# Optimization experiments

Measured on AMD Instinct MI355X. Metric: run time of the kernel, lower is better.

The kernel has to match this reference:

```python
import jax, jax.numpy as jnp
import numpy as np

B, S, D, H = 2, 2048, 2048, 16
HD = D // H  # head_dim = 128


def setup_inputs() -> dict:
    key = jax.random.key(0)
    ks = jax.random.split(key, 9)
    s = 1.0 / np.sqrt(D)
    return {
        "x": jax.random.normal(ks[0], (B, S, D), jnp.float32),
        "Wq": jax.random.normal(ks[1], (D, D), jnp.float32) * s,
        "bq": jax.random.normal(ks[2], (D,), jnp.float32) * 0.02,
        "Wk": jax.random.normal(ks[3], (D, D), jnp.float32) * s,
        "bk": jax.random.normal(ks[4], (D,), jnp.float32) * 0.02,
        "Wv": jax.random.normal(ks[5], (D, D), jnp.float32) * s,
        "bv": jax.random.normal(ks[6], (D,), jnp.float32) * 0.02,
        "Wo": jax.random.normal(ks[7], (D, D), jnp.float32) * s,
        "bo": jax.random.normal(ks[8], (D,), jnp.float32) * 0.02,
    }


def reference(x, Wq, bq, Wk, bk, Wv, bv, Wo, bo):
    b, s, d = x.shape
    # nn.Linear: y = x @ W.T + b
    def split(t):
        # [b, s, d] -> [b, H, s, HD]
        return t.reshape(b, s, H, HD).transpose(0, 2, 1, 3)

    q = split(x @ Wq.T + bq)
    k = split(x @ Wk.T + bk)
    v = split(x @ Wv.T + bv)

    scale = jnp.asarray(HD, x.dtype) ** 0.5
    qk = jnp.einsum("bhqd,bhkd->bhqk", q, k) / scale  # [b, H, s, s]
    weights = jax.nn.softmax(qk, axis=-1)
    attn = jnp.einsum("bhqk,bhkd->bhqd", weights, v)  # [b, H, s, HD]

    merged = attn.transpose(0, 2, 1, 3).reshape(b, s, d)
    return merged @ Wo.T + bo
```

## Files before the change

### kernel.cpp

```cpp
#include <hip/hip_runtime.h>

typedef __bf16 bf16_t;
typedef bf16_t bf16x8 __attribute__((ext_vector_type(8)));
typedef bf16_t bf16x4 __attribute__((ext_vector_type(4)));
typedef float  f32x4  __attribute__((ext_vector_type(4)));

#define DDIM  2048
#define SEQ   2048
#define NH    16
#define HDIM  128
#define BATCH 2
#define MROWS (BATCH * SEQ)
#define XEL   ((size_t)MROWS * DDIM)

__device__ __forceinline__ void async_ld16(const bf16_t* g, bf16_t* l) {
  __builtin_amdgcn_global_load_lds(
      (const __attribute__((address_space(1))) void*)g,
      (__attribute__((address_space(3))) void*)l, 16, 0, 0);
}

__global__ void cvt_f32_bf16(const float* __restrict__ in,
                             bf16_t* __restrict__ out, int n) {
  int i = (blockIdx.x * blockDim.x + threadIdx.x) * 4;
  const int stride = gridDim.x * blockDim.x * 4;
  for (; i < n; i += stride) {
    const float4 v = *reinterpret_cast<const float4*>(in + i);
    bf16x4 o;
    o[0] = (bf16_t)v.x; o[1] = (bf16_t)v.y;
    o[2] = (bf16_t)v.z; o[3] = (bf16_t)v.w;
    *reinterpret_cast<bf16x4*>(out + i) = o;
  }
}

__global__ __launch_bounds__(512, 2) void gemm_qkv(
    const bf16_t* __restrict__ Ax, const bf16_t* __restrict__ Wcat,
    const float* __restrict__ bq, const float* __restrict__ bk,
    const float* __restrict__ bv,
    bf16_t* __restrict__ QKVh, float qscale) {
  __shared__ __align__(16) bf16_t sA[2][2][128 * 64];
  __shared__ __align__(16) bf16_t sB[2][192 * 64];

  const int tid  = threadIdx.x;
  const int lane = tid & 63;
  const int w    = tid >> 6;
  const int wm   = w >> 2;
  const int wn   = w & 3;
  const int lg   = lane >> 4;
  const int lr   = lane & 15;

  const int bid = blockIdx.x;
  const int l   = (bid & 7) * 64 + (bid >> 3);
  const int tm  = l & 15;
  const int tn  = l >> 4;
  const int row0  = tm * 256;
  const int ncol0 = tn * 192;

  auto stA = [&](int buf, int ha, int kt) {
#pragma unroll
    for (int L = 0; L < 2; ++L) {
      const int c = L * 512 + tid, r = c >> 3, ch = c & 7;
      async_ld16(Ax + (size_t)(row0 + ha * 128 + r) * DDIM + kt * 64 +
                     ((ch ^ (r & 7)) * 8),
                 &sA[buf][ha][c * 8]);
    }
  };
  auto stB = [&](int buf, int kt) {
#pragma unroll
    for (int L = 0; L < 3; ++L) {
      const int c = L * 512 + tid, r = c >> 3, ch = c & 7;
      async_ld16(Wcat + (size_t)(ncol0 + r) * DDIM + kt * 64 +
                     ((ch ^ (r & 7)) * 8),
                 &sB[buf][c * 8]);
    }
  };
  auto ldA = [&](int buf, int mf, int k) {
    const int row = mf * 16 + lr;
    const int ch  = (k * 4 + lg) ^ (row & 7);
    return *reinterpret_cast<const bf16x8*>(&sA[buf][wm][row * 64 + ch * 8]);
  };
  auto ldB = [&](int buf, int nf, int k) {
    const int row = wn * 48 + nf * 16 + lr;
    const int ch  = (k * 4 + lg) ^ (row & 7);
    return *reinterpret_cast<const bf16x8*>(&sB[buf][row * 64 + ch * 8]);
  };

  f32x4  acc[8][3] = {};
  bf16x8 bfr[3][2];

#define GPH(BUF, Q, LOADB, STAGE_STMT, VMW)                                   \
  {                                                                           \
    bf16x8 a00 = ldA(BUF, 2 * (Q), 0), a01 = ldA(BUF, 2 * (Q), 1);            \
    bf16x8 a10 = ldA(BUF, 2 * (Q) + 1, 0), a11 = ldA(BUF, 2 * (Q) + 1, 1);    \
    if (LOADB) {                                                              \
      _Pragma("unroll") for (int nf = 0; nf < 3; ++nf) {                      \
        bfr[nf][0] = ldB(BUF, nf, 0);                                         \
        bfr[nf][1] = ldB(BUF, nf, 1);                                         \
      }                                                                       \
    }                                                                         \
    STAGE_STMT;                                                               \
    if (VMW) asm volatile("s_waitcnt vmcnt(3)" ::: "memory");                 \
    __builtin_amdgcn_s_barrier();                                             \
    asm volatile("s_waitcnt lgkmcnt(0)" ::: "memory");                        \
    __builtin_amdgcn_sched_barrier(0);                                        \
    __builtin_amdgcn_s_setprio(1);                                            \
    _Pragma("unroll") for (int k = 0; k < 2; ++k) {                           \
      const bf16x8 A0 = k ? a01 : a00;                                        \
      const bf16x8 A1 = k ? a11 : a10;                                        \
      _Pragma("unroll") for (int nf = 0; nf < 3; ++nf) {                      \
        acc[2 * (Q)][nf] = __builtin_amdgcn_mfma_f32_16x16x32_bf16(           \
            A0, bfr[nf][k], acc[2 * (Q)][nf], 0, 0, 0);                       \
        acc[2 * (Q) + 1][nf] = __builtin_amdgcn_mfma_f32_16x16x32_bf16(       \
            A1, bfr[nf][k], acc[2 * (Q) + 1][nf], 0, 0, 0);                   \
      }                                                                       \
    }                                                                         \
    __builtin_amdgcn_s_setprio(0);                                            \
    __builtin_amdgcn_s_barrier();                                             \
  }

  stA(0, 0, 0); stA(0, 1, 0);
  stB(0, 0);
  stB(1, 1);
  asm volatile("s_waitcnt vmcnt(3)" ::: "memory");
  __builtin_amdgcn_s_barrier();

  for (int i = 0; i < 16; ++i) {
    const int t1 = (2 * i + 1) & 31;
    const int t2 = (2 * i + 2) & 31;
    const int t3 = (2 * i + 3) & 31;
    GPH(0, 0, true,  { stA(1, 0, t1); stA(1, 1, t1); }, 0)
    GPH(0, 1, false, { stB(0, t2); },                   0)
    GPH(0, 2, false, {},                                0)
    GPH(0, 3, false, {},                                1)
    GPH(1, 0, true,  { stA(0, 0, t2); stA(0, 1, t2); }, 0)
    GPH(1, 1, false, { stB(1, t3); },                   0)
    GPH(1, 2, false, {},                                0)
    GPH(1, 3, false, {},                                1)
  }
#undef GPH
  asm volatile("s_waitcnt vmcnt(0)" ::: "memory");

#pragma unroll
  for (int mf = 0; mf < 8; ++mf) {
    const int rr0 = row0 + wm * 128 + mf * 16 + lg * 4;
#pragma unroll
    for (int nf = 0; nf < 3; ++nf) {
      const int col = ncol0 + wn * 48 + nf * 16 + lr;
      const int mat = col >> 11;
      const int c2  = col & (DDIM - 1);
      const float bs = ((mat == 0) ? bq : (mat == 1) ? bk : bv)[c2];
      const float sc = (mat == 0) ? qscale : 1.0f;
      const int h = c2 >> 7, hd = c2 & (HDIM - 1);
      bf16_t* outb = QKVh + (size_t)mat * XEL;
#pragma unroll
      for (int r = 0; r < 4; ++r) {
        const int rr = rr0 + r;
        const int b = rr >> 11, s = rr & (SEQ - 1);
        outb[(((size_t)(b * NH + h)) * SEQ + s) * HDIM + hd] =
            (bf16_t)((acc[mf][nf][r] + bs) * sc);
      }
    }
  }
}

template <int OUTMODE>
__global__ __launch_bounds__(256) void gemm_bt(
    const bf16_t* __restrict__ A, const bf16_t* __restrict__ Bw,
    const float* __restrict__ bias, void* __restrict__ outp,
    int M, int N, int K, float scale) {
  __shared__ __align__(16) bf16_t sA[2][128 * 32];
  __shared__ __align__(16) bf16_t sB[2][128 * 32];

  const int tid  = threadIdx.x;
  const int lane = tid & 63;
  const int w    = tid >> 6;
  const int wm   = w >> 1;
  const int wn   = w & 1;
  const int lg   = lane >> 4;
  const int lr   = lane & 15;
  const int row0 = blockIdx.y * 128;
  const int col0 = blockIdx.x * 128;

  const int srow = tid >> 2;
  const int scol = (tid & 3) * 8;

  const bf16_t* gA = A  + (size_t)(row0 + srow) * K + scol;
  const bf16_t* gB = Bw + (size_t)(col0 + srow) * K + scol;

  f32x4 acc[4][4] = {};

  auto stage = [&](int buf, int k0) {
    async_ld16(gA + k0,                  &sA[buf][tid * 8]);
    async_ld16(gA + 64 * (size_t)K + k0, &sA[buf][(256 + tid) * 8]);
    async_ld16(gB + k0,                  &sB[buf][tid * 8]);
    async_ld16(gB + 64 * (size_t)K + k0, &sB[buf][(256 + tid) * 8]);
  };

  stage(0, 0);
  __syncthreads();

  int cur = 0;
  const int NT = K / 32;
  for (int t = 0; t < NT; ++t) {
    if (t + 1 < NT) stage(cur ^ 1, (t + 1) * 32);
    bf16x8 af[4], bfr[4];
#pragma unroll
    for (int i = 0; i < 4; ++i) {
      af[i]  = *reinterpret_cast<const bf16x8*>(
          &sA[cur][(wm * 64 + i * 16 + lr) * 32 + lg * 8]);
      bfr[i] = *reinterpret_cast<const bf16x8*>(
          &sB[cur][(wn * 64 + i * 16 + lr) * 32 + lg * 8]);
    }
#pragma unroll
    for (int i = 0; i < 4; ++i)
#pragma unroll
      for (int j = 0; j < 4; ++j)
        acc[i][j] = __builtin_amdgcn_mfma_f32_16x16x32_bf16(
            af[i], bfr[j], acc[i][j], 0, 0, 0);
    __syncthreads();
    cur ^= 1;
  }

#pragma unroll
  for (int i = 0; i < 4; ++i) {
    const int rowb = row0 + wm * 64 + i * 16 + lg * 4;
#pragma unroll
    for (int j = 0; j < 4; ++j) {
      const int col = col0 + wn * 64 + j * 16 + lr;
      const float bs = bias[col];
#pragma unroll
      for (int r = 0; r < 4; ++r) {
        const float v = (acc[i][j][r] + bs) * scale;
        const int rr = rowb + r;
        if (OUTMODE == 2) {
          ((float*)outp)[(size_t)rr * N + col] = v;
        } else {
          const int b  = rr >> 11;
          const int s  = rr & (SEQ - 1);
          const int h  = col >> 7;
          const int hd = col & (HDIM - 1);
          ((bf16_t*)outp)[(((size_t)(b * NH + h)) * SEQ + s) * HDIM + hd] =
              (bf16_t)v;
        }
      }
    }
  }
}

__global__ __launch_bounds__(256) void transpose_v(
    const bf16_t* __restrict__ Vp, bf16_t* __restrict__ Vt) {
  __shared__ __align__(16) bf16_t tt[64][72];
  const int bh = blockIdx.z;
  const int s0 = blockIdx.x * 64;
  const int d0 = blockIdx.y * 64;
  const int t  = threadIdx.x;
#pragma unroll
  for (int c = 0; c < 2; ++c) {
    const int r   = (c * 256 + t) >> 3;
    const int col = (t & 7) * 8;
    bf16x8 v = *reinterpret_cast<const bf16x8*>(
        Vp + ((size_t)bh * SEQ + s0 + r) * HDIM + d0 + col);
    *reinterpret_cast<bf16x8*>(&tt[r][col]) = v;
  }
  __syncthreads();
#pragma unroll
  for (int c = 0; c < 2; ++c) {
    const int dr = (c * 256 + t) >> 3;
    const int sc = (t & 7) * 8;
    bf16x8 o;
#pragma unroll
    for (int i = 0; i < 8; ++i) o[i] = tt[sc + i][dr];
    *reinterpret_cast<bf16x8*>(
        Vt + ((size_t)bh * HDIM + d0 + dr) * SEQ + s0 + sc) = o;
  }
}

__global__ __launch_bounds__(256) void attn_fwd(
    const bf16_t* __restrict__ Q, const bf16_t* __restrict__ K,
    const bf16_t* __restrict__ Vt, bf16_t* __restrict__ out) {
  __shared__ __align__(16) bf16_t sK[64 * 128];
  __shared__ __align__(16) bf16_t sV[128 * 64];
  __shared__ __align__(16) bf16_t sP[4][32][72];

  const int tid  = threadIdx.x;
  const int lane = tid & 63;
  const int w    = tid >> 6;
  const int lg   = lane >> 4;
  const int lr   = lane & 15;

  const int bid     = blockIdx.x;
  const int logical = (bid & 7) * 64 + (bid >> 3);
  const int bh      = logical >> 4;
  const int q0      = (logical & 15) * 128;
  const int qw      = q0 + w * 32;

  const bf16_t* Kb = K  + (size_t)bh * SEQ * HDIM;
  const bf16_t* Vb = Vt + (size_t)bh * HDIM * SEQ;

  bf16x8 qf[2][4];
#pragma unroll
  for (int mf = 0; mf < 2; ++mf) {
    const bf16_t* qbase = Q + ((size_t)bh * SEQ + qw + mf * 16 + lr) * HDIM;
#pragma unroll
    for (int kc = 0; kc < 4; ++kc)
      qf[mf][kc] = *reinterpret_cast<const bf16x8*>(qbase + kc * 32 + lg * 8);
  }

  bf16x8 onesf;
#pragma unroll
  for (int i = 0; i < 8; ++i) onesf[i] = (bf16_t)1.0f;

  f32x4 o[2][8] = {};
  f32x4 o1[2] = {};

  for (int kv0 = 0; kv0 < SEQ; kv0 += 64) {
    __syncthreads();
#pragma unroll
    for (int p = 0; p < 4; ++p) {
      const int slot = p * 256 + tid;
      const int kr = slot >> 4, kc = slot & 15;
      async_ld16(Kb + ((size_t)(kv0 + kr)) * HDIM + ((kc ^ (kr & 7)) * 8),
                 sK + slot * 8);
      const int vr = slot >> 3, vc = slot & 7;
      async_ld16(Vb + (size_t)vr * SEQ + kv0 + ((vc ^ (vr & 7)) * 8),
                 sV + slot * 8);
    }
    __syncthreads();

    f32x4 s[2][4] = {};
    __builtin_amdgcn_s_setprio(1);
#pragma unroll
    for (int kc = 0; kc < 4; ++kc) {
#pragma unroll
      for (int cb = 0; cb < 4; ++cb) {
        const int r  = cb * 16 + lr;
        const int ch = kc * 4 + lg;
        bf16x8 kf = *reinterpret_cast<const bf16x8*>(
            sK + r * 128 + ((ch ^ (r & 7)) * 8));
        s[0][cb] = __builtin_amdgcn_mfma_f32_16x16x32_bf16(qf[0][kc], kf, s[0][cb], 0, 0, 0);
        s[1][cb] = __builtin_amdgcn_mfma_f32_16x16x32_bf16(qf[1][kc], kf, s[1][cb], 0, 0, 0);
      }
    }
    __builtin_amdgcn_s_setprio(0);

#pragma unroll
    for (int mf = 0; mf < 2; ++mf)
#pragma unroll
      for (int r = 0; r < 4; ++r)
#pragma unroll
        for (int cb = 0; cb < 4; ++cb) {
          const float p = __builtin_amdgcn_exp2f(s[mf][cb][r]);
          sP[w][mf * 16 + lg * 4 + r][cb * 16 + lr] = (bf16_t)p;
        }

    asm volatile("s_waitcnt lgkmcnt(0)" ::: "memory");

    __builtin_amdgcn_s_setprio(1);
#pragma unroll
    for (int ks = 0; ks < 2; ++ks) {
      bf16x8 pf0 = *reinterpret_cast<const bf16x8*>(&sP[w][lr][ks * 32 + lg * 8]);
      bf16x8 pf1 = *reinterpret_cast<const bf16x8*>(&sP[w][16 + lr][ks * 32 + lg * 8]);
      o1[0] = __builtin_amdgcn_mfma_f32_16x16x32_bf16(pf0, onesf, o1[0], 0, 0, 0);
      o1[1] = __builtin_amdgcn_mfma_f32_16x16x32_bf16(pf1, onesf, o1[1], 0, 0, 0);
#pragma unroll
      for (int ob = 0; ob < 8; ++ob) {
        const int r  = ob * 16 + lr;
        const int ch = ks * 4 + lg;
        bf16x8 vf = *reinterpret_cast<const bf16x8*>(
            sV + r * 64 + ((ch ^ (r & 7)) * 8));
        o[0][ob] = __builtin_amdgcn_mfma_f32_16x16x32_bf16(pf0, vf, o[0][ob], 0, 0, 0);
        o[1][ob] = __builtin_amdgcn_mfma_f32_16x16x32_bf16(pf1, vf, o[1][ob], 0, 0, 0);
      }
    }
    __builtin_amdgcn_s_setprio(0);
  }

  const int b = bh >> 4, h = bh & 15;
#pragma unroll
  for (int mf = 0; mf < 2; ++mf) {
#pragma unroll
    for (int r = 0; r < 4; ++r) {
      const float inv_l = 1.0f / o1[mf][r];
      const int row = qw + mf * 16 + lg * 4 + r;
      bf16_t* obase = out + ((size_t)b * SEQ + row) * DDIM + h * HDIM;
#pragma unroll
      for (int ob = 0; ob < 8; ++ob)
        obase[ob * 16 + lr] = (bf16_t)(o[mf][ob][r] * inv_l);
    }
  }
}

extern "C" void kernel_launch(void* const* d_in, const int* in_sizes, int n_in,
                              void* d_out, int out_size, void* d_ws,
                              size_t ws_size, hipStream_t stream) {
  const float* x  = (const float*)d_in[0];
  const float* Wq = (const float*)d_in[1];
  const float* bq = (const float*)d_in[2];
  const float* Wk = (const float*)d_in[3];
  const float* bk = (const float*)d_in[4];
  const float* Wv = (const float*)d_in[5];
  const float* bv = (const float*)d_in[6];
  const float* Wo = (const float*)d_in[7];
  const float* bo = (const float*)d_in[8];

  bf16_t* ws = (bf16_t*)d_ws;
  const size_t XE = XEL;
  const size_t WE = (size_t)DDIM * DDIM;
  bf16_t* xb  = ws;
  bf16_t* wqb = ws + XE;
  bf16_t* wkb = wqb + WE;
  bf16_t* wvb = wkb + WE;
  bf16_t* wob = wvb + WE;
  bf16_t* Qh  = wob + WE;
  bf16_t* Kh  = Qh + XE;
  bf16_t* Vh  = Kh + XE;
  bf16_t* Vt  = Vh + XE;
  bf16_t* merged = xb;

  cvt_f32_bf16<<<4096, 256, 0, stream>>>(x, xb, (int)XE);
  cvt_f32_bf16<<<2048, 256, 0, stream>>>(Wq, wqb, (int)WE);
  cvt_f32_bf16<<<2048, 256, 0, stream>>>(Wk, wkb, (int)WE);
  cvt_f32_bf16<<<2048, 256, 0, stream>>>(Wv, wvb, (int)WE);
  cvt_f32_bf16<<<2048, 256, 0, stream>>>(Wo, wob, (int)WE);

  const float qscale = 0.12751744520778695f;

  gemm_qkv<<<512, 512, 0, stream>>>(xb, wqb, bq, bk, bv, Qh, qscale);

  transpose_v<<<dim3(SEQ / 64, HDIM / 64, BATCH * NH), 256, 0, stream>>>(Vh, Vt);

  attn_fwd<<<512, 256, 0, stream>>>(Qh, Kh, Vt, merged);

  dim3 gg(DDIM / 128, MROWS / 128);
  gemm_bt<2><<<gg, 256, 0, stream>>>(merged, wob, bo, d_out, MROWS, DDIM, DDIM, 1.0f);
}
```

Before: 276.1 us.

## Restructure QKV GEMM main loop into one LDS read burst per K-tile

Replaces the four per-phase blocks, each with its own LDS reads and two barriers, with a single half-iteration. It issues all A and B fragment reads up front, then waits on lgkmcnt in stages so MFMA phases start while the later A fragments are still arriving. This cuts the barriers per K-tile from eight to two and hides LDS latency behind MFMA work. In exchange, 16 bf16x8 A fragments stay live at once, which raises register pressure and could lower occupancy or cause spills.

```diff
diff --git a/kernel.cpp b/kernel.cpp
--- a/kernel.cpp
+++ b/kernel.cpp
@@ -85,35 +85,54 @@
   };
 
   f32x4  acc[8][3] = {};
+  bf16x8 a[8][2];
   bf16x8 bfr[3][2];
 
-#define GPH(BUF, Q, LOADB, STAGE_STMT, VMW)                                   \
+#define MFMA_PH(Q)                                                            \
+  __builtin_amdgcn_s_setprio(1);                                              \
+  _Pragma("unroll") for (int k = 0; k < 2; ++k) {                             \
+    _Pragma("unroll") for (int nf = 0; nf < 3; ++nf) {                        \
+      acc[2 * (Q)][nf] = __builtin_amdgcn_mfma_f32_16x16x32_bf16(             \
+          a[2 * (Q)][k], bfr[nf][k], acc[2 * (Q)][nf], 0, 0, 0);              \
+      acc[2 * (Q) + 1][nf] = __builtin_amdgcn_mfma_f32_16x16x32_bf16(         \
+          a[2 * (Q) + 1][k], bfr[nf][k], acc[2 * (Q) + 1][nf], 0, 0, 0);      \
+    }                                                                         \
+  }                                                                           \
+  __builtin_amdgcn_s_setprio(0);
+
+#define HALF(BUF, ST1, ST2)                                                   \
   {                                                                           \
-    bf16x8 a00 = ldA(BUF, 2 * (Q), 0), a01 = ldA(BUF, 2 * (Q), 1);            \
-    bf16x8 a10 = ldA(BUF, 2 * (Q) + 1, 0), a11 = ldA(BUF, 2 * (Q) + 1, 1);    \
-    if (LOADB) {                                                              \
-      _Pragma("unroll") for (int nf = 0; nf < 3; ++nf) {                      \
-        bfr[nf][0] = ldB(BUF, nf, 0);                                         \
-        bfr[nf][1] = ldB(BUF, nf, 1);                                         \
-      }                                                                       \
+       \
+    a[0][0] = ldA(BUF, 0, 0); a[0][1] = ldA(BUF, 0, 1);                       \
+    a[1][0] = ldA(BUF, 1, 0); a[1][1] = ldA(BUF, 1, 1);                       \
+    _Pragma("unroll") for (int nf = 0; nf < 3; ++nf) {                        \
+      bfr[nf][0] = ldB(BUF, nf, 0); bfr[nf][1] = ldB(BUF, nf, 1);             \
     }                                                                         \
-    STAGE_STMT;                                                               \
-    if (VMW) asm volatile("s_waitcnt vmcnt(3)" ::: "memory");                 \
+    __builtin_amdgcn_sched_barrier(0);                                        \
+    a[2][0] = ldA(BUF, 2, 0); a[2][1] = ldA(BUF, 2, 1);                       \
+    a[3][0] = ldA(BUF, 3, 0); a[3][1] = ldA(BUF, 3, 1);                       \
+    __builtin_amdgcn_sched_barrier(0);                                        \
+    a[4][0] = ldA(BUF, 4, 0); a[4][1] = ldA(BUF, 4, 1);                       \
+    a[5][0] = ldA(BUF, 5, 0); a[5][1] = ldA(BUF, 5, 1);                       \
+    __builtin_amdgcn_sched_barrier(0);                                        \
+    a[6][0] = ldA(BUF, 6, 0); a[6][1] = ldA(BUF, 6, 1);                       \
+    a[7][0] = ldA(BUF, 7, 0); a[7][1] = ldA(BUF, 7, 1);                       \
+    ST1;                                                                      \
+    asm volatile("s_waitcnt lgkmcnt(12)" ::: "memory");                       \
+    __builtin_amdgcn_sched_barrier(0);                                        \
     __builtin_amdgcn_s_barrier();                                             \
+    MFMA_PH(0)                                                                \
+    ST2;                                                                      \
+    asm volatile("s_waitcnt lgkmcnt(8)" ::: "memory");                        \
+    __builtin_amdgcn_sched_barrier(0);                                        \
+    MFMA_PH(1)                                                                \
+    asm volatile("s_waitcnt lgkmcnt(4)" ::: "memory");                        \
+    __builtin_amdgcn_sched_barrier(0);                                        \
+    MFMA_PH(2)                                                                \
     asm volatile("s_waitcnt lgkmcnt(0)" ::: "memory");                        \
     __builtin_amdgcn_sched_barrier(0);                                        \
-    __builtin_amdgcn_s_setprio(1);                                            \
-    _Pragma("unroll") for (int k = 0; k < 2; ++k) {                           \
-      const bf16x8 A0 = k ? a01 : a00;                                        \
-      const bf16x8 A1 = k ? a11 : a10;                                        \
-      _Pragma("unroll") for (int nf = 0; nf < 3; ++nf) {                      \
-        acc[2 * (Q)][nf] = __builtin_amdgcn_mfma_f32_16x16x32_bf16(           \
-            A0, bfr[nf][k], acc[2 * (Q)][nf], 0, 0, 0);                       \
-        acc[2 * (Q) + 1][nf] = __builtin_amdgcn_mfma_f32_16x16x32_bf16(       \
-            A1, bfr[nf][k], acc[2 * (Q) + 1][nf], 0, 0, 0);                   \
-      }                                                                       \
-    }                                                                         \
-    __builtin_amdgcn_s_setprio(0);                                            \
+    MFMA_PH(3)                                                                \
+    asm volatile("s_waitcnt vmcnt(3)" ::: "memory");                          \
     __builtin_amdgcn_s_barrier();                                             \
   }
 
@@ -127,16 +146,11 @@
     const int t1 = (2 * i + 1) & 31;
     const int t2 = (2 * i + 2) & 31;
     const int t3 = (2 * i + 3) & 31;
-    GPH(0, 0, true,  { stA(1, 0, t1); stA(1, 1, t1); }, 0)
-    GPH(0, 1, false, { stB(0, t2); },                   0)
-    GPH(0, 2, false, {},                                0)
-    GPH(0, 3, false, {},                                1)
-    GPH(1, 0, true,  { stA(0, 0, t2); stA(0, 1, t2); }, 0)
-    GPH(1, 1, false, { stB(1, t3); },                   0)
-    GPH(1, 2, false, {},                                0)
-    GPH(1, 3, false, {},                                1)
-  }
-#undef GPH
+    HALF(0, { stA(1, 0, t1); stA(1, 1, t1); }, { stB(0, t2); })
+    HALF(1, { stA(0, 0, t2); stA(0, 1, t2); }, { stB(1, t3); })
+  }
+#undef HALF
+#undef MFMA_PH
   asm volatile("s_waitcnt vmcnt(0)" ::: "memory");
 
 #pragma unroll
```

New measurement: 252.0 us. 1.1x faster.
